# Kernel optimization log

Hardware: AMD Instinct MI355X
Metric: run time of the kernel (lower is better)

## Reference

```python
import jax, jax.numpy as jnp
import numpy as np

KH, KW = 3, 3
SH, SW = 1, 1
DH, DW = 1, 1
OFFSET_GROUPS = 1
WEIGHT_GROUPS = 1


def setup_inputs() -> dict:
    key = jax.random.key(0)
    k1, k2, k3, k4 = jax.random.split(key, 4)
    B, C, H, W = 8, 128, 64, 64
    F = 128
    x = jax.random.normal(k1, (B, C, H, W), dtype=jnp.float32)
    offset = jax.random.normal(k2, (B, OFFSET_GROUPS * 2 * KH * KW, H, W), dtype=jnp.float32)
    mask = jax.random.uniform(k3, (B, OFFSET_GROUPS * KH * KW, H, W), dtype=jnp.float32)
    weight = jax.random.normal(k4, (F, C // WEIGHT_GROUPS, KH, KW), dtype=jnp.float32) * 0.05
    return {"x": x, "offset": offset, "mask": mask, "weight": weight}


def _deform_conv2d(x, offset, mask, weight):
    B, C, H, W = x.shape
    F = weight.shape[0]
    Ho, Wo = offset.shape[2], offset.shape[3]
    KK = KH * KW
    og = OFFSET_GROUPS
    Cg = C // og

    # SAME padding (TF convention, symmetric-ish: extra pad at bottom/right)
    pad_h = max((Ho - 1) * SH + (KH - 1) * DH + 1 - H, 0)
    pad_w = max((Wo - 1) * SW + (KW - 1) * DW + 1 - W, 0)
    pad_t, pad_l = pad_h // 2, pad_w // 2

    # offsets laid out as [B, og, KK, (dy,dx), Ho, Wo]
    off = offset.reshape(B, og, KK, 2, Ho, Wo)
    dy, dx = off[:, :, :, 0], off[:, :, :, 1]  # [B, og, KK, Ho, Wo]

    ki, kj = jnp.meshgrid(jnp.arange(KH), jnp.arange(KW), indexing="ij")
    ki = ki.reshape(KK)
    kj = kj.reshape(KK)
    base_y = (jnp.arange(Ho) * SH - pad_t)[None, :] + (ki * DH)[:, None]  # [KK, Ho]
    base_x = (jnp.arange(Wo) * SW - pad_l)[None, :] + (kj * DW)[:, None]  # [KK, Wo]

    py = base_y[None, None, :, :, None].astype(x.dtype) + dy  # [B, og, KK, Ho, Wo]
    px = base_x[None, None, :, None, :].astype(x.dtype) + dx

    y0 = jnp.floor(py)
    x0 = jnp.floor(px)
    ly = py - y0  # fractional parts
    lx = px - x0
    hy = 1.0 - ly
    hx = 1.0 - lx
    y0i = y0.astype(jnp.int32)
    x0i = x0.astype(jnp.int32)

    xg = x.reshape(B, og, Cg, H * W)

    def gather_corner(yi, xi):
        valid = (yi >= 0) & (yi < H) & (xi >= 0) & (xi < W)  # [B, og, KK, Ho, Wo]
        yc = jnp.clip(yi, 0, H - 1)
        xc = jnp.clip(xi, 0, W - 1)
        flat = (yc * W + xc).reshape(B, og, 1, KK * Ho * Wo)
        vals = jnp.take_along_axis(xg, flat, axis=3).reshape(B, og, Cg, KK, Ho, Wo)
        return vals * valid[:, :, None].astype(x.dtype)

    v00 = gather_corner(y0i, x0i)
    v01 = gather_corner(y0i, x0i + 1)
    v10 = gather_corner(y0i + 1, x0i)
    v11 = gather_corner(y0i + 1, x0i + 1)

    w00 = (hy * hx)[:, :, None]
    w01 = (hy * lx)[:, :, None]
    w10 = (ly * hx)[:, :, None]
    w11 = (ly * lx)[:, :, None]
    sampled = v00 * w00 + v01 * w01 + v10 * w10 + v11 * w11  # [B, og, Cg, KK, Ho, Wo]

    # modulation mask: [B, og, KK, Ho, Wo]
    m = mask.reshape(B, og, KK, Ho, Wo)
    sampled = sampled * m[:, :, None]

    # grouped matmul (weight_groups=1 -> plain); columns ordered c*KK + kk, matching
    # weight [F, C, KH, KW] flattened.
    cols = sampled.reshape(B, C * KK, Ho, Wo)
    out = jnp.einsum("fk,bkhw->bfhw", weight.reshape(F, C // WEIGHT_GROUPS * KK), cols)
    return out


def reference(x, offset, mask, weight):
    return _deform_conv2d(x, offset, mask, weight)
```

## Files before the change

kernel.cpp:

```cpp
#include <hip/hip_runtime.h>
#include <hip/hip_bf16.h>

typedef __attribute__((ext_vector_type(8))) short bf16x8;
typedef __attribute__((ext_vector_type(4))) float f32x4;
typedef __attribute__((ext_vector_type(2))) float f32x2;
typedef unsigned int uint32;
typedef unsigned short ushort_t;
typedef __attribute__((ext_vector_type(4))) uint32 u32x4;

#define SB0() __builtin_amdgcn_sched_barrier(0)

__device__ __forceinline__ ushort_t f2bf(float f) {
    unsigned int u = __float_as_uint(f);
    u = (u + 0x7FFFu + ((u >> 16) & 1u)) >> 16;
    return (ushort_t)u;
}

__device__ __forceinline__ uint32 cvt_pk_bf16(float lo, float hi) {
    uint32 r;
    asm("v_cvt_pk_bf16_f32 %0, %1, %2" : "=v"(r) : "v"(lo), "v"(hi));
    return r;
}

__device__ __forceinline__ void gload_lds16(const void* g, void* l) {
    __builtin_amdgcn_global_load_lds(
        (const __attribute__((address_space(1))) uint32*)g,
        (__attribute__((address_space(3))) uint32*)l, 16, 0, 0);
}

__global__ __launch_bounds__(256) void prep_all(const float* __restrict__ x,
                                                const float* __restrict__ w,
                                                ushort_t* __restrict__ xt,
                                                ushort_t* __restrict__ wT2) {
    int bi = blockIdx.x;
    int t = threadIdx.x;
    if (bi >= 4096) {
        int idx = (bi - 4096) * 256 + t;
        int j  = idx & 7;
        int f  = (idx >> 3) & 127;
        int lu = (idx >> 10) & 3;
        int ks = (idx >> 12) & 3;
        int tap = idx >> 14;
        int c = ks * 32 + lu * 8 + j;
        wT2[idx] = f2bf(w[((size_t)f * 128 + c) * 9 + tap]);
        return;
    }
    __shared__ float tile[32][33];
    int b = bi & 7;
    int r2 = bi >> 3;
    int wb = r2 & 1, cb = (r2 >> 1) & 3, y = r2 >> 3;
    int lw = t & 31, lc = t >> 5;
    #pragma unroll
    for (int pass = 0; pass < 4; ++pass) {
        int c = cb * 32 + lc + pass * 8;
        tile[lc + pass * 8][lw] = x[(((size_t)b * 128 + c) * 64 + y) * 64 + wb * 32 + lw];
    }
    __syncthreads();
    int cc = t & 31, xl = t >> 5;
    #pragma unroll
    for (int pass = 0; pass < 4; ++pass) {
        int xll = xl + pass * 8;
        int xx = wb * 32 + xll;
        int c = cb * 32 + cc;
        int c2 = (((c >> 3) ^ (xx & 7)) << 3) | (c & 7);
        xt[(((size_t)b * 64 + y) * 64 + xx) * 128 + c2] = f2bf(tile[cc][xll]);
    }
}

__device__ __forceinline__ bf16x8 interp4(u32x4 c0, u32x4 c1, u32x4 c2, u32x4 c3,
                                          f32x4 wv) {
    uint32 rr[4];
    #pragma unroll
    for (int i = 0; i < 4; ++i) {
        f32x2 a, s;
        uint32 u = c0[i];
        a.x = __uint_as_float(u << 16); a.y = __uint_as_float(u & 0xffff0000u);
        s = a * wv.x;
        u = c1[i];
        a.x = __uint_as_float(u << 16); a.y = __uint_as_float(u & 0xffff0000u);
        s += a * wv.y;
        u = c2[i];
        a.x = __uint_as_float(u << 16); a.y = __uint_as_float(u & 0xffff0000u);
        s += a * wv.z;
        u = c3[i];
        a.x = __uint_as_float(u << 16); a.y = __uint_as_float(u & 0xffff0000u);
        s += a * wv.w;
        rr[i] = cvt_pk_bf16(s.x, s.y);
    }
    u32x4 q = {rr[0], rr[1], rr[2], rr[3]};
    return __builtin_bit_cast(bf16x8, q);
}

__global__ __launch_bounds__(1024, 4) void dcn_main(
    const float* __restrict__ offset, const float* __restrict__ mask,
    const ushort_t* __restrict__ xt, const ushort_t* __restrict__ wT2,
    float* __restrict__ out)
{
    __shared__ ushort_t xwin[7 * 64 * 128];
    __shared__ float  pws_l[9][64][4];
    __shared__ uint32 pos_l[9][64];

    int bi = blockIdx.x;
    int b = bi & 7, ho = bi >> 3;
    int t = threadIdx.x, lane = t & 63, wid = t >> 6;
    int pxg = wid & 3, ks = wid >> 2;
    int p = lane & 15, lu = lane >> 4;
    int px = pxg * 16 + p;
    int row0 = min(max(ho - 3, 0), 57);

    const char* xgb = (const char*)xt + (size_t)b * (64 * 64 * 256);

    {
        const char* ws = xgb + ((size_t)row0 << 14);
        #pragma unroll
        for (int r = 0; r < 7; ++r)
            gload_lds16(ws + (r * 1024 + t) * 16, (char*)xwin + (r * 1024 + t) * 16);
    }
    if (t < 576) {
        int k = t >> 6, pi = t & 63;
        int ki = k / 3, kj = k - ki * 3;
        float dy = offset[(((size_t)b * 18 + 2 * k)     * 64 + ho) * 64 + pi];
        float dx = offset[(((size_t)b * 18 + 2 * k + 1) * 64 + ho) * 64 + pi];
        float m  = mask  [(((size_t)b * 9  + k)         * 64 + ho) * 64 + pi];
        float py = (float)(ho - 1 + ki) + dy;
        float px_ = (float)(pi - 1 + kj) + dx;
        float y0f = floorf(py), x0f = floorf(px_);
        float ly = py - y0f, lx = px_ - x0f;
        float hy = 1.f - ly, hx = 1.f - lx;
        int y0 = (int)y0f, x0 = (int)x0f;
        int y1 = y0 + 1, x1 = x0 + 1;
        float vy0 = (y0 >= 0 && y0 < 64) ? 1.f : 0.f;
        float vy1 = (y1 >= 0 && y1 < 64) ? 1.f : 0.f;
        float vx0 = (x0 >= 0 && x0 < 64) ? 1.f : 0.f;
        float vx1 = (x1 >= 0 && x1 < 64) ? 1.f : 0.f;
        pws_l[k][pi][0] = hy * hx * m * vy0 * vx0;
        pws_l[k][pi][1] = hy * lx * m * vy0 * vx1;
        pws_l[k][pi][2] = ly * hx * m * vy1 * vx0;
        pws_l[k][pi][3] = ly * lx * m * vy1 * vx1;
        int y0c = min(max(y0, 0), 63), y1c = min(max(y1, 0), 63);
        int x0c = min(max(x0, 0), 63), x1c = min(max(x1, 0), 63);
        pos_l[k][pi] = (uint32)(y0c * 64 + x0c) | ((uint32)(y1c * 64 + x1c) << 16);
    }
    __syncthreads();

    f32x4 acc[8];
    #pragma unroll
    for (int i = 0; i < 8; ++i) acc[i] = (f32x4){0.f, 0.f, 0.f, 0.f};

    int klu = ks * 64 + lu * 16;
    const ushort_t* abase = wT2 + (lu * 128 + p) * 8;

    #define LOADA(DST, T)                                                      \
        do {                                                                   \
            const ushort_t* ab_ = abase + (size_t)((T) * 4 + ks) * 4096;       \
            _Pragma("unroll")                                                  \
            for (int ft_ = 0; ft_ < 8; ++ft_)                                  \
                (DST)[ft_] = *(const bf16x8*)(ab_ + ft_ * 128);                \
        } while (0)

    #define BODY(T, AR)                                                        \
        do {                                                                   \
            uint32 pp = pos_l[(T)][px];                                        \
            f32x4 wv = *(const f32x4*)pws_l[(T)][px];                          \
            int i00 = pp & 0xffffu, i11 = pp >> 16;                            \
            int y0c = i00 >> 6, x0c = i00 & 63;                                \
            int y1c = i11 >> 6, x1c = i11 & 63;                                \
            u32x4 g[4];                                                        \
            _Pragma("unroll")                                                  \
            for (int c = 0; c < 4; ++c) {                                      \
                int yc = (c < 2) ? y0c : y1c;                                  \
                int xc = (c & 1) ? x1c : x0c;                                  \
                int rl = yc - row0;                                            \
                int off = klu ^ ((xc & 7) << 4);                               \
                bool inw = (unsigned)rl < 7u;                                  \
                const char* lp = (const char*)xwin                             \
                    + (((inw ? rl : 0) * 64 + xc) << 8) + off;                 \
                g[c] = *(const u32x4*)lp;                                      \
                if (!inw) {                                                    \
                    const char* gp = xgb + (((size_t)yc * 64 + xc) << 8) + off;\
                    g[c] = *(const u32x4*)gp;                                  \
                }                                                              \
            }                                                                  \
            bf16x8 bb = interp4(g[0], g[1], g[2], g[3], wv);                   \
            _Pragma("unroll")                                                  \
            for (int ft_ = 0; ft_ < 8; ++ft_)                                  \
                acc[ft_] = __builtin_amdgcn_mfma_f32_16x16x32_bf16(            \
                    (AR)[ft_], bb, acc[ft_], 0, 0, 0);                         \
        } while (0)

    bf16x8 aP[8], aQ[8];
    LOADA(aP, 0);
    SB0();
    #pragma unroll 1
    for (int tp = 0; tp < 4; ++tp) {
        int t0 = tp * 2;
        LOADA(aQ, t0 + 1);
        SB0();
        BODY(t0, aP);
        LOADA(aP, t0 + 2);
        SB0();
        BODY(t0 + 1, aQ);
    }
    BODY(8, aP);
    #undef LOADA
    #undef BODY

    __syncthreads();
    float* red = (float*)xwin;

    #define DUMP(SLOT)                                                          \
        do {                                                                    \
            _Pragma("unroll")                                                   \
            for (int ft = 0; ft < 8; ++ft)                                      \
                _Pragma("unroll")                                               \
                for (int r = 0; r < 4; ++r)                                     \
                    red[(SLOT) * 8192 + (ft * 16 + lu * 4 + r) * 64 + px] =     \
                        acc[ft][r];                                             \
        } while (0)
    #define ADDIN(SLOT)                                                         \
        do {                                                                    \
            _Pragma("unroll")                                                   \
            for (int ft = 0; ft < 8; ++ft)                                      \
                _Pragma("unroll")                                               \
                for (int r = 0; r < 4; ++r)                                     \
                    acc[ft][r] += red[(SLOT) * 8192                             \
                        + (ft * 16 + lu * 4 + r) * 64 + px];                    \
        } while (0)

    if (ks == 1) DUMP(0);
    if (ks == 3) DUMP(1);
    __syncthreads();
    if (ks == 0) ADDIN(0);
    if (ks == 2) ADDIN(1);
    __syncthreads();
    if (ks == 2) DUMP(0);
    __syncthreads();
    if (ks == 0) {
        ADDIN(0);
        float* outb = out + (size_t)b * 128 * 4096 + ho * 64;
        #pragma unroll
        for (int ft = 0; ft < 8; ++ft)
            #pragma unroll
            for (int r = 0; r < 4; ++r) {
                int f = ft * 16 + lu * 4 + r;
                outb[(size_t)f * 4096 + px] = acc[ft][r];
            }
    }
    #undef DUMP
    #undef ADDIN
}

extern "C" void kernel_launch(void* const* d_in, const int* in_sizes, int n_in,
                              void* d_out, int out_size, void* d_ws, size_t ws_size,
                              hipStream_t stream) {
    const float* x      = (const float*)d_in[0];
    const float* offset = (const float*)d_in[1];
    const float* mask   = (const float*)d_in[2];
    const float* weight = (const float*)d_in[3];
    float* out = (float*)d_out;

    ushort_t* xt  = (ushort_t*)d_ws;
    ushort_t* wT2 = xt + (size_t)8 * 64 * 64 * 128;
    if (ws_size < (size_t)(8 * 64 * 64 * 128 + 9 * 16384) * 2) return;

    prep_all<<<4672, 256, 0, stream>>>(x, weight, xt, wT2);
    dcn_main<<<512, 1024, 0, stream>>>(offset, mask, xt, wT2, out);
}
```

Baseline: 45.13 us.

## Widen LDS input window to nine rows and restructure gather/MFMA pipeline

Grows the staged LDS input window from 7 to 9 rows so fewer bilinear samples fall back to global memory. The tap loop now gathers two taps from LDS up front, patches out-of-window samples from global afterwards, and reloads weight fragments inline per MFMA rather than double-buffering them in registers. The reduction scratch gets a row stride of 65 to avoid LDS bank conflicts. In exchange, LDS use rises (about 144KB for xwin), which may limit residency, and dropping the register prefetch of weights may expose global load latency.

```diff
diff --git a/kernel.cpp b/kernel.cpp
--- a/kernel.cpp
+++ b/kernel.cpp
@@ -7,8 +7,6 @@
 typedef unsigned int uint32;
 typedef unsigned short ushort_t;
 typedef __attribute__((ext_vector_type(4))) uint32 u32x4;
-
-#define SB0() __builtin_amdgcn_sched_barrier(0)
 
 __device__ __forceinline__ ushort_t f2bf(float f) {
     unsigned int u = __float_as_uint(f);
@@ -96,7 +94,7 @@
     const ushort_t* __restrict__ xt, const ushort_t* __restrict__ wT2,
     float* __restrict__ out)
 {
-    __shared__ ushort_t xwin[7 * 64 * 128];
+    __shared__ ushort_t xwin[9 * 64 * 128];
     __shared__ float  pws_l[9][64][4];
     __shared__ uint32 pos_l[9][64];
 
@@ -106,14 +104,14 @@
     int pxg = wid & 3, ks = wid >> 2;
     int p = lane & 15, lu = lane >> 4;
     int px = pxg * 16 + p;
-    int row0 = min(max(ho - 3, 0), 57);
+    int row0 = min(max(ho - 4, 0), 55);
 
     const char* xgb = (const char*)xt + (size_t)b * (64 * 64 * 256);
 
     {
         const char* ws = xgb + ((size_t)row0 << 14);
         #pragma unroll
-        for (int r = 0; r < 7; ++r)
+        for (int r = 0; r < 9; ++r)
             gload_lds16(ws + (r * 1024 + t) * 16, (char*)xwin + (r * 1024 + t) * 16);
     }
     if (t < 576) {
@@ -150,60 +148,75 @@
     int klu = ks * 64 + lu * 16;
     const ushort_t* abase = wT2 + (lu * 128 + p) * 8;
 
-    #define LOADA(DST, T)                                                      \
-        do {                                                                   \
-            const ushort_t* ab_ = abase + (size_t)((T) * 4 + ks) * 4096;       \
-            _Pragma("unroll")                                                  \
-            for (int ft_ = 0; ft_ < 8; ++ft_)                                  \
-                (DST)[ft_] = *(const bf16x8*)(ab_ + ft_ * 128);                \
-        } while (0)
-
-    #define BODY(T, AR)                                                        \
+    #define GATHER_LDS(T, G, REC)                                              \
         do {                                                                   \
             uint32 pp = pos_l[(T)][px];                                        \
-            f32x4 wv = *(const f32x4*)pws_l[(T)][px];                          \
             int i00 = pp & 0xffffu, i11 = pp >> 16;                            \
             int y0c = i00 >> 6, x0c = i00 & 63;                                \
             int y1c = i11 >> 6, x1c = i11 & 63;                                \
-            u32x4 g[4];                                                        \
             _Pragma("unroll")                                                  \
             for (int c = 0; c < 4; ++c) {                                      \
                 int yc = (c < 2) ? y0c : y1c;                                  \
                 int xc = (c & 1) ? x1c : x0c;                                  \
                 int rl = yc - row0;                                            \
                 int off = klu ^ ((xc & 7) << 4);                               \
-                bool inw = (unsigned)rl < 7u;                                  \
+                (REC)[c] = (uint32)(((yc * 64 + xc) << 8) + off)               \
+                           | (((unsigned)rl < 9u) ? 0x80000000u : 0u);         \
                 const char* lp = (const char*)xwin                             \
-                    + (((inw ? rl : 0) * 64 + xc) << 8) + off;                 \
-                g[c] = *(const u32x4*)lp;                                      \
-                if (!inw) {                                                    \
-                    const char* gp = xgb + (((size_t)yc * 64 + xc) << 8) + off;\
-                    g[c] = *(const u32x4*)gp;                                  \
+                    + ((((unsigned)rl < 9u ? rl : 0) * 64 + xc) << 8) + off;   \
+                (G)[c] = *(const u32x4*)lp;                                    \
+            }                                                                  \
+        } while (0)
+
+    #define GATHER_FIX(G, REC)                                                 \
+        do {                                                                   \
+            _Pragma("unroll")                                                  \
+            for (int c = 0; c < 4; ++c) {                                      \
+                if (!((REC)[c] & 0x80000000u)) {                               \
+                    (G)[c] = *(const u32x4*)(xgb + ((REC)[c] & 0x7fffffffu));  \
                 }                                                              \
             }                                                                  \
-            bf16x8 bb = interp4(g[0], g[1], g[2], g[3], wv);                   \
+        } while (0)
+
+    #define MFMA8(T, BB)                                                       \
+        do {                                                                   \
+            const ushort_t* ab_ = abase + (size_t)((T) * 4 + ks) * 4096;       \
             _Pragma("unroll")                                                  \
-            for (int ft_ = 0; ft_ < 8; ++ft_)                                  \
+            for (int ft_ = 0; ft_ < 8; ++ft_) {                                \
+                bf16x8 aa = *(const bf16x8*)(ab_ + ft_ * 128);                 \
                 acc[ft_] = __builtin_amdgcn_mfma_f32_16x16x32_bf16(            \
-                    (AR)[ft_], bb, acc[ft_], 0, 0, 0);                         \
-        } while (0)
-
-    bf16x8 aP[8], aQ[8];
-    LOADA(aP, 0);
-    SB0();
+                    aa, (BB), acc[ft_], 0, 0, 0);                              \
+            }                                                                  \
+        } while (0)
+
     #pragma unroll 1
-    for (int tp = 0; tp < 4; ++tp) {
-        int t0 = tp * 2;
-        LOADA(aQ, t0 + 1);
-        SB0();
-        BODY(t0, aP);
-        LOADA(aP, t0 + 2);
-        SB0();
-        BODY(t0 + 1, aQ);
-    }
-    BODY(8, aP);
-    #undef LOADA
-    #undef BODY
+    for (int pr = 0; pr < 4; ++pr) {
+        int t0 = pr * 2;
+        u32x4 g0[4], g1[4];
+        uint32 rec0[4], rec1[4];
+        GATHER_LDS(t0, g0, rec0);
+        GATHER_LDS(t0 + 1, g1, rec1);
+        GATHER_FIX(g0, rec0);
+        GATHER_FIX(g1, rec1);
+        f32x4 wv0 = *(const f32x4*)pws_l[t0][px];
+        f32x4 wv1 = *(const f32x4*)pws_l[t0 + 1][px];
+        bf16x8 b0 = interp4(g0[0], g0[1], g0[2], g0[3], wv0);
+        bf16x8 b1 = interp4(g1[0], g1[1], g1[2], g1[3], wv1);
+        MFMA8(t0, b0);
+        MFMA8(t0 + 1, b1);
+    }
+    {
+        u32x4 g0[4];
+        uint32 rec0[4];
+        GATHER_LDS(8, g0, rec0);
+        GATHER_FIX(g0, rec0);
+        f32x4 wv0 = *(const f32x4*)pws_l[8][px];
+        bf16x8 b0 = interp4(g0[0], g0[1], g0[2], g0[3], wv0);
+        MFMA8(8, b0);
+    }
+    #undef GATHER_LDS
+    #undef GATHER_FIX
+    #undef MFMA8
 
     __syncthreads();
     float* red = (float*)xwin;
@@ -214,7 +227,7 @@
             for (int ft = 0; ft < 8; ++ft)                                      \
                 _Pragma("unroll")                                               \
                 for (int r = 0; r < 4; ++r)                                     \
-                    red[(SLOT) * 8192 + (ft * 16 + lu * 4 + r) * 64 + px] =     \
+                    red[(SLOT) * 8320 + (ft * 16 + lu * 4 + r) * 65 + px] =     \
                         acc[ft][r];                                             \
         } while (0)
     #define ADDIN(SLOT)                                                         \
@@ -223,8 +236,8 @@
             for (int ft = 0; ft < 8; ++ft)                                      \
                 _Pragma("unroll")                                               \
                 for (int r = 0; r < 4; ++r)                                     \
-                    acc[ft][r] += red[(SLOT) * 8192                             \
-                        + (ft * 16 + lu * 4 + r) * 64 + px];                    \
+                    acc[ft][r] += red[(SLOT) * 8320                             \
+                        + (ft * 16 + lu * 4 + r) * 65 + px];                    \
         } while (0)
 
     if (ks == 1) DUMP(0);
```

Result: faster. 41.33 us, median of 2 (-8.4%).
